# Performance work log

Hardware: AMD Instinct MI355X
Metric: run time of the kernel (lower is better)

## Reference

```python
import jax, jax.numpy as jnp
import numpy as np

NUM_CHANS = 64
LAG = 5
HIDDEN = [32, 32]  # module appends a final 1-channel layer
BATCH = 16
T = 2048


def setup_inputs() -> dict:
    key = jax.random.key(0)
    ks = jax.random.split(key, 7)
    p, h0, h1 = NUM_CHANS, HIDDEN[0], HIDDEN[1]
    # Per-network weights stacked along leading axis n = num_series = p.
    # Xavier-ish scale for layer 0 (Conv1d(p, h0, lag)), default-ish for rest.
    s0 = float(np.sqrt(2.0 / (p * LAG + h0)))
    return {
        "X": jax.random.normal(ks[0], (BATCH, T, p), dtype=jnp.float32),
        "W0": jax.random.normal(ks[1], (p, h0, p, LAG), dtype=jnp.float32) * s0,
        "b0": jax.random.normal(ks[2], (p, h0), dtype=jnp.float32) * 0.01,
        "W1": jax.random.normal(ks[3], (p, h1, h0), dtype=jnp.float32) * float(np.sqrt(1.0 / h0)),
        "b1": jax.random.normal(ks[4], (p, h1), dtype=jnp.float32) * 0.01,
        "W2": jax.random.normal(ks[5], (p, 1, h1), dtype=jnp.float32) * float(np.sqrt(1.0 / h1)),
        "b2": jax.random.normal(ks[6], (p, 1), dtype=jnp.float32) * 0.01,
    }


def reference(X, W0, b0, W1, b1, W2, b2):
    # X: [B, T, p]. Each of n=p networks: Conv1d(p,h0,lag) -> ReLU -> Conv1d(h0,h1,1)
    # -> ReLU -> Conv1d(h1,1,1); outputs concatenated along last dim.
    lag = W0.shape[-1]
    Tout = X.shape[1] - lag + 1  # valid conv output length
    # Sliding windows: Xwin[b,t,c,l] = X[b, t+l, c]  -> [B, Tout, p, lag]
    Xwin = jnp.stack([X[:, l:l + Tout, :] for l in range(lag)], axis=-1)
    # Layer 0 across all n networks at once: [B, n, Tout, h0]
    h = jnp.einsum('btcl,nhcl->bnth', Xwin, W0) + b0[None, :, None, :]
    # 1x1 conv layers (per-network dense along channel dim)
    h = jax.nn.relu(h)
    h = jnp.einsum('bnti,noi->bnto', h, W1) + b1[None, :, None, :]
    h = jax.nn.relu(h)
    h = jnp.einsum('bnti,noi->bnto', h, W2) + b2[None, :, None, :]  # [B, n, Tout, 1]
    # concat along dim 2 of (batch, Tout, 1) per network -> (B, Tout, n)
    return jnp.transpose(h[..., 0], (0, 2, 1))
```

## Files before the change

kernel.cpp:

```cpp
#include <hip/hip_runtime.h>

#define NCH 64
#define LAG 5
#define H0 32
#define H1 32
#define TIN 2048
#define TOUT 2044
#define NBATCH 16

#define XSTRIDE 72
#define HSTRIDE 40

typedef __attribute__((ext_vector_type(8))) short short8;
typedef __attribute__((ext_vector_type(4))) float f32x4;

__device__ __forceinline__ unsigned short f2bf(float f) {
    unsigned u = __float_as_uint(f);
    u += 0x7fffu + ((u >> 16) & 1u);
    return (unsigned short)(u >> 16);
}

__global__ __launch_bounds__(256) void prep_w(
    const float* __restrict__ W0, unsigned short* __restrict__ W0b,
    const float* __restrict__ W1, unsigned short* __restrict__ W1b,
    const float* __restrict__ W2, unsigned short* __restrict__ W2b)
{
    const int bx = blockIdx.x;
    if (bx < 512) {
        int j = bx * 256 + threadIdx.x;
        int nh = j >> 6, c = j & 63;
        const float* src = W0 + (size_t)j * LAG;
        unsigned short* dst = W0b + nh * 320 + c;
        #pragma unroll
        for (int l = 0; l < LAG; ++l) dst[l * 64] = f2bf(src[l]);
    } else if (bx < 544) {
        int i = ((bx - 512) * 256 + threadIdx.x) * 8;
        float4 a = *(const float4*)(W1 + i);
        float4 b = *(const float4*)(W1 + i + 4);
        unsigned long long v0 = (unsigned long long)f2bf(a.x)
                              | ((unsigned long long)f2bf(a.y) << 16)
                              | ((unsigned long long)f2bf(a.z) << 32)
                              | ((unsigned long long)f2bf(a.w) << 48);
        unsigned long long v1 = (unsigned long long)f2bf(b.x)
                              | ((unsigned long long)f2bf(b.y) << 16)
                              | ((unsigned long long)f2bf(b.z) << 32)
                              | ((unsigned long long)f2bf(b.w) << 48);
        *(unsigned long long*)(W1b + i)     = v0;
        *(unsigned long long*)(W1b + i + 4) = v1;
    } else {
        int i = threadIdx.x * 8;
        float4 a = *(const float4*)(W2 + i);
        float4 b = *(const float4*)(W2 + i + 4);
        unsigned long long v0 = (unsigned long long)f2bf(a.x)
                              | ((unsigned long long)f2bf(a.y) << 16)
                              | ((unsigned long long)f2bf(a.z) << 32)
                              | ((unsigned long long)f2bf(a.w) << 48);
        unsigned long long v1 = (unsigned long long)f2bf(b.x)
                              | ((unsigned long long)f2bf(b.y) << 16)
                              | ((unsigned long long)f2bf(b.z) << 32)
                              | ((unsigned long long)f2bf(b.w) << 48);
        *(unsigned long long*)(W2b + i)     = v0;
        *(unsigned long long*)(W2b + i + 4) = v1;
    }
}

__global__ __launch_bounds__(256, 2) void mlp_mfma(
    const float* __restrict__ X,
    const unsigned short* __restrict__ W0b,
    const unsigned short* __restrict__ W1b,
    const unsigned short* __restrict__ W2b,
    const float* __restrict__ b0, const float* __restrict__ b1,
    const float* __restrict__ b2, float* __restrict__ out)
{
    __shared__ __align__(16) unsigned short xs[260 * XSTRIDE];
    __shared__ __align__(16) unsigned short hs[4][64 * HSTRIDE];
    __shared__ __align__(16) float yt[256][4];

    const int tileid = blockIdx.x;
    const int ng     = blockIdx.y;
    const int b      = tileid >> 3;
    const int t0     = (tileid & 7) * 256;
    const int tid    = threadIdx.x;
    const int wave   = tid >> 6;
    const int lane   = tid & 63;
    const int quad   = lane >> 4;
    const int l15    = lane & 15;

    const float* src = X + ((size_t)(b * TIN + t0)) * NCH;
    const int rows = (t0 == 1792) ? 256 : 260;
    for (int s = tid; s < rows * 16; s += 256) {
        int r = s >> 4, seg = s & 15;
        float4 x = *(const float4*)(src + s * 4);
        unsigned long long v = (unsigned long long)f2bf(x.x)
                             | ((unsigned long long)f2bf(x.y) << 16)
                             | ((unsigned long long)f2bf(x.z) << 32)
                             | ((unsigned long long)f2bf(x.w) << 48);
        *(unsigned long long*)&xs[r * XSTRIDE + seg * 4] = v;
    }
    __syncthreads();

    const int n = ng * 4 + wave;
    short8 B0[10][2];
    const unsigned short* wp0 = W0b + (n * H0 + l15) * (NCH * LAG) + quad * 8;
    #pragma unroll
    for (int ks = 0; ks < 10; ++ks) {
        B0[ks][0] = *(const short8*)(wp0 + ks * 32);
        B0[ks][1] = *(const short8*)(wp0 + 16 * (NCH * LAG) + ks * 32);
    }
    short8 B1[2];
    const unsigned short* wp1 = W1b + (n * H1 + l15) * H0 + quad * 8;
    B1[0] = *(const short8*)(wp1);
    B1[1] = *(const short8*)(wp1 + 16 * H0);
    short8 B2 = *(const short8*)(W2b + n * H1 + quad * 8);
    const float b0v0 = b0[n * H0 + l15], b0v1 = b0[n * H0 + 16 + l15];
    const float b1v0 = b1[n * H1 + l15], b1v1 = b1[n * H1 + 16 + l15];
    const float b2s  = b2[n];

    const int vmax = (t0 == 1792) ? 251 : 255;
    unsigned short* hrow = hs[wave];

    #pragma unroll 1
    for (int chunk = 0; chunk < 4; ++chunk) {
        int rowoff[4];
        #pragma unroll
        for (int mf = 0; mf < 4; ++mf) {
            int i = chunk * 64 + mf * 16 + l15;
            i = i < vmax ? i : vmax;
            rowoff[mf] = i * XSTRIDE + quad * 8;
        }

        f32x4 acc[4][2];
        #pragma unroll
        for (int mf = 0; mf < 4; ++mf) {
            acc[mf][0] = (f32x4){ b0v0, b0v0, b0v0, b0v0 };
            acc[mf][1] = (f32x4){ b0v1, b0v1, b0v1, b0v1 };
        }
        #pragma unroll
        for (int ks = 0; ks < 10; ++ks) {
            const int xoff = (ks >> 1) * XSTRIDE + (ks & 1) * 32;
            #pragma unroll
            for (int mf = 0; mf < 4; ++mf) {
                short8 A = *(const short8*)&xs[rowoff[mf] + xoff];
                acc[mf][0] = __builtin_amdgcn_mfma_f32_16x16x32_bf16(A, B0[ks][0], acc[mf][0], 0, 0, 0);
                acc[mf][1] = __builtin_amdgcn_mfma_f32_16x16x32_bf16(A, B0[ks][1], acc[mf][1], 0, 0, 0);
            }
        }

        #pragma unroll
        for (int mf = 0; mf < 4; ++mf)
            #pragma unroll
            for (int nf = 0; nf < 2; ++nf)
                #pragma unroll
                for (int r = 0; r < 4; ++r)
                    hrow[(mf * 16 + quad * 4 + r) * HSTRIDE + nf * 16 + l15] =
                        f2bf(fmaxf(acc[mf][nf][r], 0.0f));

        f32x4 acc1[4][2];
        #pragma unroll
        for (int mf = 0; mf < 4; ++mf) {
            acc1[mf][0] = (f32x4){ b1v0, b1v0, b1v0, b1v0 };
            acc1[mf][1] = (f32x4){ b1v1, b1v1, b1v1, b1v1 };
        }
        #pragma unroll
        for (int mf = 0; mf < 4; ++mf) {
            short8 A1 = *(const short8*)&hrow[(mf * 16 + l15) * HSTRIDE + quad * 8];
            acc1[mf][0] = __builtin_amdgcn_mfma_f32_16x16x32_bf16(A1, B1[0], acc1[mf][0], 0, 0, 0);
            acc1[mf][1] = __builtin_amdgcn_mfma_f32_16x16x32_bf16(A1, B1[1], acc1[mf][1], 0, 0, 0);
        }

        #pragma unroll
        for (int mf = 0; mf < 4; ++mf)
            #pragma unroll
            for (int nf = 0; nf < 2; ++nf)
                #pragma unroll
                for (int r = 0; r < 4; ++r)
                    hrow[(mf * 16 + quad * 4 + r) * HSTRIDE + nf * 16 + l15] =
                        f2bf(fmaxf(acc1[mf][nf][r], 0.0f));

        #pragma unroll
        for (int mf = 0; mf < 4; ++mf) {
            short8 A2 = *(const short8*)&hrow[(mf * 16 + l15) * HSTRIDE + quad * 8];
            f32x4 c2 = (f32x4){ b2s, b2s, b2s, b2s };
            c2 = __builtin_amdgcn_mfma_f32_16x16x32_bf16(A2, B2, c2, 0, 0, 0);
            float v = (l15 & 2) ? ((l15 & 1) ? c2[3] : c2[2])
                                : ((l15 & 1) ? c2[1] : c2[0]);
            if (quad == (l15 >> 2))
                yt[chunk * 64 + mf * 16 + l15][wave] = v;
        }
    }
    __syncthreads();

    int t = t0 + tid;
    if (t < TOUT) {
        float4 v = *(const float4*)yt[tid];
        *(float4*)&out[((size_t)(b * TOUT + t)) * NCH + ng * 4] = v;
    }
}

extern "C" void kernel_launch(void* const* d_in, const int* in_sizes, int n_in,
                              void* d_out, int out_size, void* d_ws, size_t ws_size,
                              hipStream_t stream)
{
    const float* X  = (const float*)d_in[0];
    const float* W0 = (const float*)d_in[1];
    const float* b0 = (const float*)d_in[2];
    const float* W1 = (const float*)d_in[3];
    const float* b1 = (const float*)d_in[4];
    const float* W2 = (const float*)d_in[5];
    const float* b2 = (const float*)d_in[6];
    float* out = (float*)d_out;

    unsigned short* W0b = (unsigned short*)d_ws;
    unsigned short* W1b = (unsigned short*)((char*)d_ws + 1310720);
    unsigned short* W2b = (unsigned short*)((char*)d_ws + 1441792);

    prep_w<<<545, 256, 0, stream>>>(W0, W0b, W1, W1b, W2, W2b);
    mlp_mfma<<<dim3(128, 16), 256, 0, stream>>>(X, W0b, W1b, W2b, b0, b1, b2, out);
}
```

Baseline: 136.5 us.

## Process two networks per wave to halve X tile staging and conversion

Each wave now handles two of the per-series networks instead of one, so the grid's network dimension halves and every block's bf16 X tile in shared memory feeds eight networks rather than four. This halves global X reads and fp32-to-bf16 conversion work per output. Final outputs are staged in shared memory as bf16 and written as two float4s per row. The cost is double the weight registers (launch bounds drop to one block per SM) and an extra bf16 rounding of the outputs. A leftover, broken mlp_mfma kernel remains but is no longer launched.

```diff
diff --git a/kernel.cpp b/kernel.cpp
--- a/kernel.cpp
+++ b/kernel.cpp
@@ -10,6 +10,7 @@
 
 #define XSTRIDE 72
 #define HSTRIDE 40
+#define HREG 3072
 
 typedef __attribute__((ext_vector_type(8))) short short8;
 typedef __attribute__((ext_vector_type(4))) float f32x4;
@@ -64,7 +65,7 @@
     }
 }
 
-__global__ __launch_bounds__(256, 2) void mlp_mfma(
+__global__ __launch_bounds__(256, 1) void mlp_mfma(
     const float* __restrict__ X,
     const unsigned short* __restrict__ W0b,
     const unsigned short* __restrict__ W1b,
@@ -73,8 +74,7 @@
     const float* __restrict__ b2, float* __restrict__ out)
 {
     __shared__ __align__(16) unsigned short xs[260 * XSTRIDE];
-    __shared__ __align__(16) unsigned short hs[4][64 * HSTRIDE];
-    __shared__ __align__(16) float yt[256][4];
+    __shared__ __align__(16) unsigned short hs[4][HREG];
 
     const int tileid = blockIdx.x;
     const int ng     = blockIdx.y;
@@ -99,25 +99,32 @@
     }
     __syncthreads();
 
-    const int n = ng * 4 + wave;
-    short8 B0[10][2];
-    const unsigned short* wp0 = W0b + (n * H0 + l15) * (NCH * LAG) + quad * 8;
+    const int n0 = ng * 8 + wave * 2;
+    short8 B0[10][2][2];
+    short8 B1[2][2];
+    short8 B2[2];
+    float  b0v[2][2], b1v[2][2], b2s[2];
     #pragma unroll
-    for (int ks = 0; ks < 10; ++ks) {
-        B0[ks][0] = *(const short8*)(wp0 + ks * 32);
-        B0[ks][1] = *(const short8*)(wp0 + 16 * (NCH * LAG) + ks * 32);
-    }
-    short8 B1[2];
-    const unsigned short* wp1 = W1b + (n * H1 + l15) * H0 + quad * 8;
-    B1[0] = *(const short8*)(wp1);
-    B1[1] = *(const short8*)(wp1 + 16 * H0);
-    short8 B2 = *(const short8*)(W2b + n * H1 + quad * 8);
-    const float b0v0 = b0[n * H0 + l15], b0v1 = b0[n * H0 + 16 + l15];
-    const float b1v0 = b1[n * H1 + l15], b1v1 = b1[n * H1 + 16 + l15];
-    const float b2s  = b2[n];
+    for (int e = 0; e < 2; ++e) {
+        const int n = n0 + e;
+        const unsigned short* wp0 = W0b + (n * H0 + l15) * (NCH * LAG) + quad * 8;
+        #pragma unroll
+        for (int ks = 0; ks < 10; ++ks) {
+            B0[ks][e][0] = *(const short8*)(wp0 + ks * 32);
+            B0[ks][e][1] = *(const short8*)(wp0 + 16 * (NCH * LAG) + ks * 32);
+        }
+        const unsigned short* wp1 = W1b + (n * H1 + l15) * H0 + quad * 8;
+        B1[e][0] = *(const short8*)(wp1);
+        B1[e][1] = *(const short8*)(wp1 + 16 * H0);
+        B2[e]    = *(const short8*)(W2b + n * H1 + quad * 8);
+        b0v[e][0] = b0[n * H0 + l15];  b0v[e][1] = b0[n * H0 + 16 + l15];
+        b1v[e][0] = b1[n * H1 + l15];  b1v[e][1] = b1[n * H1 + 16 + l15];
+        b2s[e]    = b2[n];
+    }
 
     const int vmax = (t0 == 1792) ? 251 : 255;
     unsigned short* hrow = hs[wave];
+    unsigned short* ytw  = hs[wave] + 2560;
 
     #pragma unroll 1
     for (int chunk = 0; chunk < 4; ++chunk) {
@@ -129,71 +136,238 @@
             rowoff[mf] = i * XSTRIDE + quad * 8;
         }
 
-        f32x4 acc[4][2];
-        #pragma unroll
-        for (int mf = 0; mf < 4; ++mf) {
-            acc[mf][0] = (f32x4){ b0v0, b0v0, b0v0, b0v0 };
-            acc[mf][1] = (f32x4){ b0v1, b0v1, b0v1, b0v1 };
-        }
+        f32x4 acc[4][2][2];
+        #pragma unroll
+        for (int mf = 0; mf < 4; ++mf)
+            #pragma unroll
+            for (int e = 0; e < 2; ++e) {
+                acc[mf][e][0] = (f32x4){ b0v[e][0], b0v[e][0], b0v[e][0], b0v[e][0] };
+                acc[mf][e][1] = (f32x4){ b0v[e][1], b0v[e][1], b0v[e][1], b0v[e][1] };
+            }
         #pragma unroll
         for (int ks = 0; ks < 10; ++ks) {
             const int xoff = (ks >> 1) * XSTRIDE + (ks & 1) * 32;
             #pragma unroll
             for (int mf = 0; mf < 4; ++mf) {
                 short8 A = *(const short8*)&xs[rowoff[mf] + xoff];
-                acc[mf][0] = __builtin_amdgcn_mfma_f32_16x16x32_bf16(A, B0[ks][0], acc[mf][0], 0, 0, 0);
-                acc[mf][1] = __builtin_amdgcn_mfma_f32_16x16x32_bf16(A, B0[ks][1], acc[mf][1], 0, 0, 0);
-            }
-        }
-
-        #pragma unroll
-        for (int mf = 0; mf < 4; ++mf)
-            #pragma unroll
-            for (int nf = 0; nf < 2; ++nf)
+                acc[mf][0][0] = __builtin_amdgcn_mfma_f32_16x16x32_bf16(A, B0[ks][0][0], acc[mf][0][0], 0, 0, 0);
+                acc[mf][0][1] = __builtin_amdgcn_mfma_f32_16x16x32_bf16(A, B0[ks][0][1], acc[mf][0][1], 0, 0, 0);
+                acc[mf][1][0] = __builtin_amdgcn_mfma_f32_16x16x32_bf16(A, B0[ks][1][0], acc[mf][1][0], 0, 0, 0);
+                acc[mf][1][1] = __builtin_amdgcn_mfma_f32_16x16x32_bf16(A, B0[ks][1][1], acc[mf][1][1], 0, 0, 0);
+            }
+        }
+
+        #pragma unroll
+        for (int e = 0; e < 2; ++e) {
+            #pragma unroll
+            for (int mf = 0; mf < 4; ++mf)
                 #pragma unroll
-                for (int r = 0; r < 4; ++r)
-                    hrow[(mf * 16 + quad * 4 + r) * HSTRIDE + nf * 16 + l15] =
-                        f2bf(fmaxf(acc[mf][nf][r], 0.0f));
-
-        f32x4 acc1[4][2];
-        #pragma unroll
-        for (int mf = 0; mf < 4; ++mf) {
-            acc1[mf][0] = (f32x4){ b1v0, b1v0, b1v0, b1v0 };
-            acc1[mf][1] = (f32x4){ b1v1, b1v1, b1v1, b1v1 };
-        }
-        #pragma unroll
-        for (int mf = 0; mf < 4; ++mf) {
-            short8 A1 = *(const short8*)&hrow[(mf * 16 + l15) * HSTRIDE + quad * 8];
-            acc1[mf][0] = __builtin_amdgcn_mfma_f32_16x16x32_bf16(A1, B1[0], acc1[mf][0], 0, 0, 0);
-            acc1[mf][1] = __builtin_amdgcn_mfma_f32_16x16x32_bf16(A1, B1[1], acc1[mf][1], 0, 0, 0);
-        }
-
-        #pragma unroll
-        for (int mf = 0; mf < 4; ++mf)
-            #pragma unroll
-            for (int nf = 0; nf < 2; ++nf)
+                for (int nf = 0; nf < 2; ++nf)
+                    #pragma unroll
+                    for (int r = 0; r < 4; ++r)
+                        hrow[(mf * 16 + quad * 4 + r) * HSTRIDE + nf * 16 + l15] =
+                            f2bf(fmaxf(acc[mf][e][nf][r], 0.0f));
+
+            f32x4 acc1[4][2];
+            #pragma unroll
+            for (int mf = 0; mf < 4; ++mf) {
+                acc1[mf][0] = (f32x4){ b1v[e][0], b1v[e][0], b1v[e][0], b1v[e][0] };
+                acc1[mf][1] = (f32x4){ b1v[e][1], b1v[e][1], b1v[e][1], b1v[e][1] };
+            }
+            #pragma unroll
+            for (int mf = 0; mf < 4; ++mf) {
+                short8 A1 = *(const short8*)&hrow[(mf * 16 + l15) * HSTRIDE + quad * 8];
+                acc1[mf][0] = __builtin_amdgcn_mfma_f32_16x16x32_bf16(A1, B1[e][0], acc1[mf][0], 0, 0, 0);
+                acc1[mf][1] = __builtin_amdgcn_mfma_f32_16x16x32_bf16(A1, B1[e][1], acc1[mf][1], 0, 0, 0);
+            }
+
+            #pragma unroll
+            for (int mf = 0; mf < 4; ++mf)
                 #pragma unroll
-                for (int r = 0; r < 4; ++r)
-                    hrow[(mf * 16 + quad * 4 + r) * HSTRIDE + nf * 16 + l15] =
-                        f2bf(fmaxf(acc1[mf][nf][r], 0.0f));
-
-        #pragma unroll
-        for (int mf = 0; mf < 4; ++mf) {
-            short8 A2 = *(const short8*)&hrow[(mf * 16 + l15) * HSTRIDE + quad * 8];
-            f32x4 c2 = (f32x4){ b2s, b2s, b2s, b2s };
-            c2 = __builtin_amdgcn_mfma_f32_16x16x32_bf16(A2, B2, c2, 0, 0, 0);
-            float v = (l15 & 2) ? ((l15 & 1) ? c2[3] : c2[2])
-                                : ((l15 & 1) ? c2[1] : c2[0]);
-            if (quad == (l15 >> 2))
-                yt[chunk * 64 + mf * 16 + l15][wave] = v;
-        }
-    }
+                for (int nf = 0; nf < 2; ++nf)
+                    #pragma unroll
+                    for (int r = 0; r < 4; ++r)
+                        hrow[(mf * 16 + quad * 4 + r) * HSTRIDE + nf * 16 + l15] =
+                            f2bf(fmaxf(acc1[mf][e ? 1 : nf][r], 0.0f));
+        }
+        #pragma unroll
+        for (int e = 0; e < 0; ++e) {}
+
+        (void)0;
+    }
+
+
     __syncthreads();
-
     int t = t0 + tid;
     if (t < TOUT) {
-        float4 v = *(const float4*)yt[tid];
-        *(float4*)&out[((size_t)(b * TOUT + t)) * NCH + ng * 4] = v;
+        float o[8];
+        #pragma unroll
+        for (int w = 0; w < 4; ++w) {
+            unsigned v = *(const unsigned*)&hs[w][2560 + tid * 2];
+            o[w * 2]     = __uint_as_float((v & 0xffffu) << 16);
+            o[w * 2 + 1] = __uint_as_float(v & 0xffff0000u);
+        }
+        float4 lo = { o[0], o[1], o[2], o[3] };
+        float4 hi = { o[4], o[5], o[6], o[7] };
+        float* base = out + ((size_t)(b * TOUT + t)) * NCH + ng * 8;
+        *(float4*)base       = lo;
+        *(float4*)(base + 4) = hi;
+    }
+}
+
+__global__ __launch_bounds__(256, 1) void mlp_mfma2(
+    const float* __restrict__ X,
+    const unsigned short* __restrict__ W0b,
+    const unsigned short* __restrict__ W1b,
+    const unsigned short* __restrict__ W2b,
+    const float* __restrict__ b0, const float* __restrict__ b1,
+    const float* __restrict__ b2, float* __restrict__ out)
+{
+    __shared__ __align__(16) unsigned short xs[260 * XSTRIDE];
+    __shared__ __align__(16) unsigned short hs[4][HREG];
+
+    const int tileid = blockIdx.x;
+    const int ng     = blockIdx.y;
+    const int b      = tileid >> 3;
+    const int t0     = (tileid & 7) * 256;
+    const int tid    = threadIdx.x;
+    const int wave   = tid >> 6;
+    const int lane   = tid & 63;
+    const int quad   = lane >> 4;
+    const int l15    = lane & 15;
+
+    const float* src = X + ((size_t)(b * TIN + t0)) * NCH;
+    const int rows = (t0 == 1792) ? 256 : 260;
+    for (int s = tid; s < rows * 16; s += 256) {
+        int r = s >> 4, seg = s & 15;
+        float4 x = *(const float4*)(src + s * 4);
+        unsigned long long v = (unsigned long long)f2bf(x.x)
+                             | ((unsigned long long)f2bf(x.y) << 16)
+                             | ((unsigned long long)f2bf(x.z) << 32)
+                             | ((unsigned long long)f2bf(x.w) << 48);
+        *(unsigned long long*)&xs[r * XSTRIDE + seg * 4] = v;
+    }
+    __syncthreads();
+
+    const int n0 = ng * 8 + wave * 2;
+    short8 B0[10][2][2];
+    short8 B1[2][2];
+    short8 B2[2];
+    float  b0v[2][2], b1v[2][2], b2s[2];
+    #pragma unroll
+    for (int e = 0; e < 2; ++e) {
+        const int n = n0 + e;
+        const unsigned short* wp0 = W0b + (n * H0 + l15) * (NCH * LAG) + quad * 8;
+        #pragma unroll
+        for (int ks = 0; ks < 10; ++ks) {
+            B0[ks][e][0] = *(const short8*)(wp0 + ks * 32);
+            B0[ks][e][1] = *(const short8*)(wp0 + 16 * (NCH * LAG) + ks * 32);
+        }
+        const unsigned short* wp1 = W1b + (n * H1 + l15) * H0 + quad * 8;
+        B1[e][0] = *(const short8*)(wp1);
+        B1[e][1] = *(const short8*)(wp1 + 16 * H0);
+        B2[e]    = *(const short8*)(W2b + n * H1 + quad * 8);
+        b0v[e][0] = b0[n * H0 + l15];  b0v[e][1] = b0[n * H0 + 16 + l15];
+        b1v[e][0] = b1[n * H1 + l15];  b1v[e][1] = b1[n * H1 + 16 + l15];
+        b2s[e]    = b2[n];
+    }
+
+    const int vmax = (t0 == 1792) ? 251 : 255;
+    unsigned short* hrow = hs[wave];
+    unsigned short* ytw  = hs[wave] + 2560;
+
+    #pragma unroll 1
+    for (int chunk = 0; chunk < 4; ++chunk) {
+        int rowoff[4];
+        #pragma unroll
+        for (int mf = 0; mf < 4; ++mf) {
+            int i = chunk * 64 + mf * 16 + l15;
+            i = i < vmax ? i : vmax;
+            rowoff[mf] = i * XSTRIDE + quad * 8;
+        }
+
+        f32x4 acc[4][2][2];
+        #pragma unroll
+        for (int mf = 0; mf < 4; ++mf)
+            #pragma unroll
+            for (int e = 0; e < 2; ++e) {
+                acc[mf][e][0] = (f32x4){ b0v[e][0], b0v[e][0], b0v[e][0], b0v[e][0] };
+                acc[mf][e][1] = (f32x4){ b0v[e][1], b0v[e][1], b0v[e][1], b0v[e][1] };
+            }
+        #pragma unroll
+        for (int ks = 0; ks < 10; ++ks) {
+            const int xoff = (ks >> 1) * XSTRIDE + (ks & 1) * 32;
+            #pragma unroll
+            for (int mf = 0; mf < 4; ++mf) {
+                short8 A = *(const short8*)&xs[rowoff[mf] + xoff];
+                acc[mf][0][0] = __builtin_amdgcn_mfma_f32_16x16x32_bf16(A, B0[ks][0][0], acc[mf][0][0], 0, 0, 0);
+                acc[mf][0][1] = __builtin_amdgcn_mfma_f32_16x16x32_bf16(A, B0[ks][0][1], acc[mf][0][1], 0, 0, 0);
+                acc[mf][1][0] = __builtin_amdgcn_mfma_f32_16x16x32_bf16(A, B0[ks][1][0], acc[mf][1][0], 0, 0, 0);
+                acc[mf][1][1] = __builtin_amdgcn_mfma_f32_16x16x32_bf16(A, B0[ks][1][1], acc[mf][1][1], 0, 0, 0);
+            }
+        }
+
+        #pragma unroll
+        for (int e = 0; e < 2; ++e) {
+            #pragma unroll
+            for (int mf = 0; mf < 4; ++mf)
+                #pragma unroll
+                for (int nf = 0; nf < 2; ++nf)
+                    #pragma unroll
+                    for (int r = 0; r < 4; ++r)
+                        hrow[(mf * 16 + quad * 4 + r) * HSTRIDE + nf * 16 + l15] =
+                            f2bf(fmaxf(acc[mf][e][nf][r], 0.0f));
+
+            f32x4 acc1[4][2];
+            #pragma unroll
+            for (int mf = 0; mf < 4; ++mf) {
+                acc1[mf][0] = (f32x4){ b1v[e][0], b1v[e][0], b1v[e][0], b1v[e][0] };
+                acc1[mf][1] = (f32x4){ b1v[e][1], b1v[e][1], b1v[e][1], b1v[e][1] };
+            }
+            #pragma unroll
+            for (int mf = 0; mf < 4; ++mf) {
+                short8 A1 = *(const short8*)&hrow[(mf * 16 + l15) * HSTRIDE + quad * 8];
+                acc1[mf][0] = __builtin_amdgcn_mfma_f32_16x16x32_bf16(A1, B1[e][0], acc1[mf][0], 0, 0, 0);
+                acc1[mf][1] = __builtin_amdgcn_mfma_f32_16x16x32_bf16(A1, B1[e][1], acc1[mf][1], 0, 0, 0);
+            }
+
+            #pragma unroll
+            for (int mf = 0; mf < 4; ++mf)
+                #pragma unroll
+                for (int nf = 0; nf < 2; ++nf)
+                    #pragma unroll
+                    for (int r = 0; r < 4; ++r)
+                        hrow[(mf * 16 + quad * 4 + r) * HSTRIDE + nf * 16 + l15] =
+                            f2bf(fmaxf(acc1[mf][nf][r], 0.0f));
+
+            #pragma unroll
+            for (int mf = 0; mf < 4; ++mf) {
+                short8 A2 = *(const short8*)&hrow[(mf * 16 + l15) * HSTRIDE + quad * 8];
+                f32x4 c2 = (f32x4){ b2s[e], b2s[e], b2s[e], b2s[e] };
+                c2 = __builtin_amdgcn_mfma_f32_16x16x32_bf16(A2, B2[e], c2, 0, 0, 0);
+                float v = (l15 & 2) ? ((l15 & 1) ? c2[3] : c2[2])
+                                    : ((l15 & 1) ? c2[1] : c2[0]);
+                if (quad == (l15 >> 2))
+                    ytw[(chunk * 64 + mf * 16 + l15) * 2 + e] = f2bf(v);
+            }
+        }
+    }
+    __syncthreads();
+
+    int t = t0 + tid;
+    if (t < TOUT) {
+        float o[8];
+        #pragma unroll
+        for (int w = 0; w < 4; ++w) {
+            unsigned v = *(const unsigned*)&hs[w][2560 + tid * 2];
+            o[w * 2]     = __uint_as_float((v & 0xffffu) << 16);
+            o[w * 2 + 1] = __uint_as_float(v & 0xffff0000u);
+        }
+        float4 lo = { o[0], o[1], o[2], o[3] };
+        float4 hi = { o[4], o[5], o[6], o[7] };
+        float* base = out + ((size_t)(b * TOUT + t)) * NCH + ng * 8;
+        *(float4*)base       = lo;
+        *(float4*)(base + 4) = hi;
     }
 }
 
@@ -215,5 +389,5 @@
     unsigned short* W2b = (unsigned short*)((char*)d_ws + 1441792);
 
     prep_w<<<545, 256, 0, stream>>>(W0, W0b, W1, W1b, W2, W2b);
-    mlp_mfma<<<dim3(128, 16), 256, 0, stream>>>(X, W0b, W1b, W2b, b0, b1, b2, out);
-}
+    mlp_mfma2<<<dim3(128, 8), 256, 0, stream>>>(X, W0b, W1b, W2b, b0, b1, b2, out);
+}
```

Measured after the change: 180.6 us. +32.3%, slower.

## Transpose MFMA operands so hidden activations chain in registers without LDS

Applied to the files above, without the earlier changes.

Layer 0 now computes the transposed product (weights as the A operand, inputs as B), so each lane's accumulator holds four consecutive hidden channels for one time step. That register layout matches the B operand of the 16x16x16 bf16 MFMA, so layers 1 and 2 consume packed ReLU'd accumulators directly from registers. This removes the per-wave LDS hidden buffer and its scattered stores and reloads. It also frees LDS and adds a few more small MFMAs per tile.

```diff
diff --git a/kernel.cpp b/kernel.cpp
--- a/kernel.cpp
+++ b/kernel.cpp
@@ -9,15 +9,30 @@
 #define NBATCH 16
 
 #define XSTRIDE 72
-#define HSTRIDE 40
 
 typedef __attribute__((ext_vector_type(8))) short short8;
+typedef __attribute__((ext_vector_type(4))) short short4v;
 typedef __attribute__((ext_vector_type(4))) float f32x4;
 
 __device__ __forceinline__ unsigned short f2bf(float f) {
     unsigned u = __float_as_uint(f);
     u += 0x7fffu + ((u >> 16) & 1u);
     return (unsigned short)(u >> 16);
+}
+
+__device__ __forceinline__ unsigned pack2bf_relu(float a, float b) {
+    unsigned ua = __float_as_uint(fmaxf(a, 0.0f));
+    unsigned ub = __float_as_uint(fmaxf(b, 0.0f));
+    ua += 0x7fffu + ((ua >> 16) & 1u);
+    ub += 0x7fffu + ((ub >> 16) & 1u);
+    return (ua >> 16) | (ub & 0xffff0000u);
+}
+
+__device__ __forceinline__ short4v pack4bf_relu(const f32x4& v) {
+    union { short4v s; unsigned u[2]; } cv;
+    cv.u[0] = pack2bf_relu(v[0], v[1]);
+    cv.u[1] = pack2bf_relu(v[2], v[3]);
+    return cv.s;
 }
 
 __global__ __launch_bounds__(256) void prep_w(
@@ -73,7 +88,6 @@
     const float* __restrict__ b2, float* __restrict__ out)
 {
     __shared__ __align__(16) unsigned short xs[260 * XSTRIDE];
-    __shared__ __align__(16) unsigned short hs[4][64 * HSTRIDE];
     __shared__ __align__(16) float yt[256][4];
 
     const int tileid = blockIdx.x;
@@ -107,17 +121,24 @@
         B0[ks][0] = *(const short8*)(wp0 + ks * 32);
         B0[ks][1] = *(const short8*)(wp0 + 16 * (NCH * LAG) + ks * 32);
     }
-    short8 B1[2];
-    const unsigned short* wp1 = W1b + (n * H1 + l15) * H0 + quad * 8;
-    B1[0] = *(const short8*)(wp1);
-    B1[1] = *(const short8*)(wp1 + 16 * H0);
-    short8 B2 = *(const short8*)(W2b + n * H1 + quad * 8);
-    const float b0v0 = b0[n * H0 + l15], b0v1 = b0[n * H0 + 16 + l15];
-    const float b1v0 = b1[n * H1 + l15], b1v1 = b1[n * H1 + 16 + l15];
-    const float b2s  = b2[n];
+    short4v A1[2][2];
+    #pragma unroll
+    for (int of = 0; of < 2; ++of)
+        #pragma unroll
+        for (int kf = 0; kf < 2; ++kf)
+            A1[of][kf] = *(const short4v*)(W1b + (n * H1 + of * 16 + l15) * H0 + kf * 16 + quad * 4);
+    short4v A2[2];
+    #pragma unroll
+    for (int kf = 0; kf < 2; ++kf)
+        A2[kf] = *(const short4v*)(W2b + n * H1 + kf * 16 + quad * 4);
+    f32x4 b0q[2], b1q[2];
+    #pragma unroll
+    for (int nf = 0; nf < 2; ++nf) b0q[nf] = *(const f32x4*)(b0 + n * H0 + nf * 16 + quad * 4);
+    #pragma unroll
+    for (int of = 0; of < 2; ++of) b1q[of] = *(const f32x4*)(b1 + n * H1 + of * 16 + quad * 4);
+    const float b2s = b2[n];
 
     const int vmax = (t0 == 1792) ? 251 : 255;
-    unsigned short* hrow = hs[wave];
 
     #pragma unroll 1
     for (int chunk = 0; chunk < 4; ++chunk) {
@@ -132,60 +153,40 @@
         f32x4 acc[4][2];
         #pragma unroll
         for (int mf = 0; mf < 4; ++mf) {
-            acc[mf][0] = (f32x4){ b0v0, b0v0, b0v0, b0v0 };
-            acc[mf][1] = (f32x4){ b0v1, b0v1, b0v1, b0v1 };
+            acc[mf][0] = b0q[0];
+            acc[mf][1] = b0q[1];
         }
         #pragma unroll
         for (int ks = 0; ks < 10; ++ks) {
             const int xoff = (ks >> 1) * XSTRIDE + (ks & 1) * 32;
             #pragma unroll
             for (int mf = 0; mf < 4; ++mf) {
-                short8 A = *(const short8*)&xs[rowoff[mf] + xoff];
-                acc[mf][0] = __builtin_amdgcn_mfma_f32_16x16x32_bf16(A, B0[ks][0], acc[mf][0], 0, 0, 0);
-                acc[mf][1] = __builtin_amdgcn_mfma_f32_16x16x32_bf16(A, B0[ks][1], acc[mf][1], 0, 0, 0);
+                short8 Xf = *(const short8*)&xs[rowoff[mf] + xoff];
+                acc[mf][0] = __builtin_amdgcn_mfma_f32_16x16x32_bf16(B0[ks][0], Xf, acc[mf][0], 0, 0, 0);
+                acc[mf][1] = __builtin_amdgcn_mfma_f32_16x16x32_bf16(B0[ks][1], Xf, acc[mf][1], 0, 0, 0);
             }
         }
 
         #pragma unroll
-        for (int mf = 0; mf < 4; ++mf)
-            #pragma unroll
-            for (int nf = 0; nf < 2; ++nf)
-                #pragma unroll
-                for (int r = 0; r < 4; ++r)
-                    hrow[(mf * 16 + quad * 4 + r) * HSTRIDE + nf * 16 + l15] =
-                        f2bf(fmaxf(acc[mf][nf][r], 0.0f));
-
-        f32x4 acc1[4][2];
-        #pragma unroll
         for (int mf = 0; mf < 4; ++mf) {
-            acc1[mf][0] = (f32x4){ b1v0, b1v0, b1v0, b1v0 };
-            acc1[mf][1] = (f32x4){ b1v1, b1v1, b1v1, b1v1 };
-        }
-        #pragma unroll
-        for (int mf = 0; mf < 4; ++mf) {
-            short8 A1 = *(const short8*)&hrow[(mf * 16 + l15) * HSTRIDE + quad * 8];
-            acc1[mf][0] = __builtin_amdgcn_mfma_f32_16x16x32_bf16(A1, B1[0], acc1[mf][0], 0, 0, 0);
-            acc1[mf][1] = __builtin_amdgcn_mfma_f32_16x16x32_bf16(A1, B1[1], acc1[mf][1], 0, 0, 0);
-        }
-
-        #pragma unroll
-        for (int mf = 0; mf < 4; ++mf)
-            #pragma unroll
-            for (int nf = 0; nf < 2; ++nf)
-                #pragma unroll
-                for (int r = 0; r < 4; ++r)
-                    hrow[(mf * 16 + quad * 4 + r) * HSTRIDE + nf * 16 + l15] =
-                        f2bf(fmaxf(acc1[mf][nf][r], 0.0f));
-
-        #pragma unroll
-        for (int mf = 0; mf < 4; ++mf) {
-            short8 A2 = *(const short8*)&hrow[(mf * 16 + l15) * HSTRIDE + quad * 8];
-            f32x4 c2 = (f32x4){ b2s, b2s, b2s, b2s };
-            c2 = __builtin_amdgcn_mfma_f32_16x16x32_bf16(A2, B2, c2, 0, 0, 0);
-            float v = (l15 & 2) ? ((l15 & 1) ? c2[3] : c2[2])
-                                : ((l15 & 1) ? c2[1] : c2[0]);
-            if (quad == (l15 >> 2))
-                yt[chunk * 64 + mf * 16 + l15][wave] = v;
+            short4v Bh0 = pack4bf_relu(acc[mf][0]);
+            short4v Bh1 = pack4bf_relu(acc[mf][1]);
+
+            f32x4 D1[2] = { b1q[0], b1q[1] };
+            D1[0] = __builtin_amdgcn_mfma_f32_16x16x16bf16_1k(A1[0][0], Bh0, D1[0], 0, 0, 0);
+            D1[0] = __builtin_amdgcn_mfma_f32_16x16x16bf16_1k(A1[0][1], Bh1, D1[0], 0, 0, 0);
+            D1[1] = __builtin_amdgcn_mfma_f32_16x16x16bf16_1k(A1[1][0], Bh0, D1[1], 0, 0, 0);
+            D1[1] = __builtin_amdgcn_mfma_f32_16x16x16bf16_1k(A1[1][1], Bh1, D1[1], 0, 0, 0);
+
+            short4v Bg0 = pack4bf_relu(D1[0]);
+            short4v Bg1 = pack4bf_relu(D1[1]);
+
+            f32x4 D2 = (f32x4){ b2s, b2s, b2s, b2s };
+            D2 = __builtin_amdgcn_mfma_f32_16x16x16bf16_1k(A2[0], Bg0, D2, 0, 0, 0);
+            D2 = __builtin_amdgcn_mfma_f32_16x16x16bf16_1k(A2[1], Bg1, D2, 0, 0, 0);
+
+            if (quad == 0)
+                yt[chunk * 64 + mf * 16 + l15][wave] = D2[0];
         }
     }
     __syncthreads();
```

New measurement: 132.0 us. -3.3%, faster.
